# Kernel tuning notes

Hardware: AMD Instinct MI355X
Metric: run time of the kernel (lower is better)

## Reference

```python
import jax, jax.numpy as jnp
import numpy as np

K = 2            # negative:positive edge ratio (init arg k)
N_NODES = 4096
N_EDGES = 8192
FEAT = 64


def setup_inputs() -> dict:
    key = jax.random.key(0)
    k1, k2, k3 = jax.random.split(key, 3)
    node_feature = jax.random.normal(k1, (N_NODES, FEAT), dtype=jnp.float32)
    edge_src = jax.random.randint(k2, (N_EDGES,), 0, N_NODES, dtype=jnp.int32)
    edge_dst = jax.random.randint(k3, (N_EDGES,), 0, N_NODES, dtype=jnp.int32)
    return {"node_feature": node_feature, "edge_src": edge_src, "edge_dst": edge_dst}


def reference(node_feature, edge_src, edge_dst):
    E = edge_src.shape[0]
    N = node_feature.shape[0]
    # [E, E] pairwise mask: candidate column j is valid for row i iff
    # dst[j] != dst[i] and dst[j] != src[i]
    valid = (edge_dst[:, None] != edge_dst[None, :]) & (edge_src[:, None] != edge_dst[None, :])
    # unsorted_segment_min over rows grouped by edge_src -> [N, E]
    segmin = jax.ops.segment_min(valid.astype(jnp.int8), edge_src, num_segments=N)
    # gather back per edge -> [E, E], flatten
    m = segmin[edge_src].reshape(-1).astype(bool)  # [E*E]
    num_negatives = jnp.sum(m)
    ratio = num_negatives // E                      # integer ratio as in TF code
    keep_prob = (K / ratio).astype(jnp.float32)
    u = jax.random.uniform(jax.random.key(42), (E * E,), dtype=jnp.float32)
    keep = m & (u < keep_prob)
    # fixed-size (jit-friendly) stand-in for tf.boolean_mask: expected count is K*E;
    # pad/truncate to exactly K*E kept flat indices (fill_value=0 pads).
    idx = jnp.nonzero(keep, size=K * E, fill_value=0)[0]
    rows = idx // E
    cols = idx % E
    edge_src_neg = edge_src[rows]
    edge_dst_neg = edge_dst[cols]
    return edge_src_neg, edge_dst_neg
```

## Files before the change

### kernel.cpp

```cpp
#include <hip/hip_runtime.h>
#include <stdint.h>
#include <math.h>

typedef unsigned int u32;
typedef unsigned long long u64;

#define E_CNT   8192
#define N_CNT   4096
#define TOT_N   (1u << 26)
#define OUT_K   16384
#define NODE_BM_WORDS 128
#define N_BLKS  8192

#define OFF_BAD      0x000000
#define OFF_CNT_DST  0x200000
#define OFF_CNT_SRC  0x204000
#define OFF_SCALARS  0x208000
#define OFF_DESC     0x210000
#define ZERO_BYTES   0x220000

__device__ __forceinline__ u32 rotl32(u32 x, u32 d) {
  return __builtin_amdgcn_alignbit(x, x, 32u - d);
}

__device__ __forceinline__ u32 mbcnt64(u64 m) {
  return __builtin_amdgcn_mbcnt_hi((u32)(m >> 32),
         __builtin_amdgcn_mbcnt_lo((u32)m, 0u));
}

__device__ __forceinline__ void threefry4_0_42(u32 ia, u32 ib, u32 ic, u32 id,
                                               u32& ra, u32& rb, u32& rc, u32& rd) {
  const u32 k1 = 42u, k2 = 0x1BD11BF0u;
  u32 A0 = 0u, A1 = ia + k1;
  u32 B0 = 0u, B1 = ib + k1;
  u32 C0 = 0u, C1 = ic + k1;
  u32 D0 = 0u, D1 = id + k1;
#define R4(r) { A0 += A1; B0 += B1; C0 += C1; D0 += D1; \
  A1 = rotl32(A1, r); B1 = rotl32(B1, r); C1 = rotl32(C1, r); D1 = rotl32(D1, r); \
  A1 ^= A0; B1 ^= B0; C1 ^= C0; D1 ^= D0; }
#define INJ(c0, c1) { A0 += (c0); B0 += (c0); C0 += (c0); D0 += (c0); \
  A1 += (c1); B1 += (c1); C1 += (c1); D1 += (c1); }
#define INJ1(c1) { A1 += (c1); B1 += (c1); C1 += (c1); D1 += (c1); }
  R4(13) R4(15) R4(26) R4(6)
  INJ(k1, k2 + 1u)
  R4(17) R4(29) R4(16) R4(24)
  INJ(k2, 2u)
  R4(13) R4(15) R4(26) R4(6)
  INJ1(k1 + 3u)
  R4(17) R4(29) R4(16) R4(24)
  INJ(k1, k2 + 4u)
  R4(13) R4(15) R4(26) R4(6)
  INJ(k2, 5u)
#undef R4
#undef INJ
#undef INJ1
  ra = A0 ^ A1;
  rb = B0 ^ B1;
  rc = C0 ^ C1;
  rd = D0 ^ D1;
}

__global__ void k_build(const int* __restrict__ src, const int* __restrict__ dst,
                        u32* __restrict__ bad, u32* __restrict__ cnt_dst,
                        u32* __restrict__ cnt_src) {
  int tid = blockIdx.x * 256 + threadIdx.x;
  if (tid < N_CNT) {
    atomicOr(&bad[(u32)tid * NODE_BM_WORDS + ((u32)tid >> 5)], 1u << (tid & 31));
  }
  u32 s = (u32)src[tid], d = (u32)dst[tid];
  atomicOr(&bad[s * NODE_BM_WORDS + (d >> 5)], 1u << (d & 31));
  atomicAdd(&cnt_dst[d], 1u);
  atomicAdd(&cnt_src[s], 1u);
}

__global__ void __launch_bounds__(1024) k_rowcount(const u32* __restrict__ bad,
                                                   const u32* __restrict__ cnt_dst,
                                                   const u32* __restrict__ cnt_src,
                                                   u32* __restrict__ scal) {
  int wv = threadIdx.x >> 6, ln = threadIdx.x & 63;
  int n = blockIdx.x * 16 + wv;
  const u32* row = bad + (u32)n * NODE_BM_WORDS;
  u32 sum = 0;
#pragma unroll
  for (int h = 0; h < 2; ++h) {
    int w = ln + h * 64;
    u32 bits = row[w];
    while (bits) { int b = __ffs(bits) - 1; sum += cnt_dst[(w << 5) + b]; bits &= bits - 1; }
  }
#pragma unroll
  for (int off = 32; off > 0; off >>= 1) sum += __shfl_down(sum, off, 64);
  __shared__ u32 part[16];
  if (ln == 0) part[wv] = ((u32)E_CNT - sum) * cnt_src[n];
  __syncthreads();
  if (threadIdx.x == 0) {
    u32 tot = 0;
#pragma unroll
    for (int k = 0; k < 16; ++k) tot += part[k];
    atomicAdd(&scal[0], tot);
    __threadfence();
    if (atomicAdd(&scal[1], 1u) == 255u) {
      u32 nn = atomicAdd(&scal[0], 0u);
      u32 ratio = nn >> 13;
      float kp = 2.0f / (float)ratio;
      u32 T = (u32)ceil((double)kp * 8388608.0);
      u32 T9 = (T >= (1u << 23)) ? 0xFFFFFFFFu : (T << 9);
      atomicExch(&scal[2], T9);
    }
  }
}

__global__ void __launch_bounds__(1024) k_sample(const int* __restrict__ src,
                                                 const int* __restrict__ dst,
                                                 const u32* __restrict__ bad,
                                                 u32* __restrict__ scal,
                                                 u64* __restrict__ desc,
                                                 int* __restrict__ out) {
  __shared__ u32 sh_cnt[16];
  __shared__ u32 sh_vb;
  __shared__ u32 sh_excl;
  const u32 t = threadIdx.x;
  const u32 wv = t >> 6, ln = t & 63;

  if (t == 0) sh_vb = atomicAdd(&scal[3], 1u);
  __syncthreads();
  const u32 vb = sh_vb;
  const u32 T9 = scal[2];
  const u32 i0w = vb * 8192u + wv * 512u;

  u64 words[8];
  u64 any = 0;
#pragma unroll
  for (int h = 0; h < 2; ++h) {
    u32 i0 = i0w + (u32)h * 256u + ln;
    u32 b0, b1, b2, b3;
    threefry4_0_42(i0, i0 + 64u, i0 + 128u, i0 + 192u, b0, b1, b2, b3);
    u64 m0 = __ballot(b0 < T9);
    u64 m1 = __ballot(b1 < T9);
    u64 m2 = __ballot(b2 < T9);
    u64 m3 = __ballot(b3 < T9);
    words[4 * h]     = m0;
    words[4 * h + 1] = m1;
    words[4 * h + 2] = m2;
    words[4 * h + 3] = m3;
    any |= m0 | m1 | m2 | m3;
  }
  if (any) {
#pragma unroll
    for (int k = 0; k < 8; ++k) {
      if (words[k]) {
        u32 i = i0w + (u32)k * 64u + ln;
        bool kp = (words[k] >> ln) & 1ull;
        if (kp) {
          u32 n = (u32)src[i >> 13]; u32 v = (u32)dst[i & 8191];
          kp = ((bad[n * NODE_BM_WORDS + (v >> 5)] >> (v & 31)) & 1u) == 0u;
        }
        words[k] = __ballot(kp);
      }
    }
  }
  u32 wcnt = 0;
#pragma unroll
  for (int k = 0; k < 8; ++k) wcnt += (u32)__popcll(words[k]);
  if (ln == 0) sh_cnt[wv] = wcnt;
  __syncthreads();

  if (wv == 0) {
    u32 tot = 0;
#pragma unroll
    for (int k = 0; k < 16; ++k) tot += sh_cnt[k];
    if (ln == 0) atomicExch(&desc[vb], (1ull << 32) | (u64)tot);
    u32 excl = 0;
    if (vb != 0u) {
      int base = (int)vb - 1;
      for (;;) {
        int idx = base - (int)ln;
        u64 d = (idx >= 0) ? atomicAdd(&desc[idx], 0ull) : (2ull << 32);
        u32 flag = (u32)(d >> 32);
        u64 incl_m = __ballot(flag == 2u);
        u64 nr_m   = __ballot(flag == 0u);
        int fi = incl_m ? (__ffsll((unsigned long long)incl_m) - 1) : 64;
        int fn = nr_m   ? (__ffsll((unsigned long long)nr_m)   - 1) : 64;
        if (fn < fi) { __builtin_amdgcn_s_sleep(1); continue; }
        u32 contrib = ((int)ln <= fi) ? (u32)d : 0u;
#pragma unroll
        for (int off = 32; off > 0; off >>= 1) contrib += __shfl_down(contrib, off, 64);
        excl += __shfl(contrib, 0, 64);
        if (fi < 64) break;
        base -= 64;
        if (base < 0) break;
      }
    }
    if (ln == 0) {
      atomicExch(&desc[vb], (2ull << 32) | (u64)(excl + tot));
      sh_excl = excl;
    }
  }
  __syncthreads();

  u32 wexcl = sh_excl;
#pragma unroll
  for (int k = 0; k < 16; ++k) wexcl += ((u32)k < wv) ? sh_cnt[k] : 0u;
  u32 rbase = wexcl;
#pragma unroll
  for (int k = 0; k < 8; ++k) {
    u64 wk = words[k];
    if ((wk >> ln) & 1ull) {
      u32 rank = rbase + mbcnt64(wk);
      if (rank < OUT_K) {
        u32 i = i0w + (u32)k * 64u + ln;
        out[rank]         = src[i >> 13];
        out[OUT_K + rank] = dst[i & 8191];
      }
    }
    rbase += (u32)__popcll(wk);
  }

  if (vb == (u32)(N_BLKS - 1)) {
    u32 tot = 0;
#pragma unroll
    for (int k = 0; k < 16; ++k) tot += sh_cnt[k];
    u32 total = sh_excl + tot;
    int s0 = src[0], d0 = dst[0];
    for (u32 p = total + t; p < OUT_K; p += 1024u) {
      out[p] = s0; out[OUT_K + p] = d0;
    }
  }
}

extern "C" void kernel_launch(void* const* d_in, const int* in_sizes, int n_in,
                              void* d_out, int out_size, void* d_ws, size_t ws_size,
                              hipStream_t stream) {
  const int* src = (const int*)d_in[1];
  const int* dst = (const int*)d_in[2];
  int* out = (int*)d_out;
  char* ws = (char*)d_ws;

  u32* bad     = (u32*)(ws + OFF_BAD);
  u32* cnt_dst = (u32*)(ws + OFF_CNT_DST);
  u32* cnt_src = (u32*)(ws + OFF_CNT_SRC);
  u32* scal    = (u32*)(ws + OFF_SCALARS);
  u64* desc    = (u64*)(ws + OFF_DESC);

  hipMemsetAsync(ws, 0, ZERO_BYTES, stream);
  k_build<<<E_CNT / 256, 256, 0, stream>>>(src, dst, bad, cnt_dst, cnt_src);
  k_rowcount<<<N_CNT / 16, 1024, 0, stream>>>(bad, cnt_dst, cnt_src, scal);
  k_sample<<<N_BLKS, 1024, 0, stream>>>(src, dst, bad, scal, desc, out);
}
```

Measured before the change: 223.2 us.

## Fuse build and rowcount kernels via grid barrier; widen decoupled look-back to full block

Merges the bitmap/count build kernel and the row-count kernel into one launch of 256 blocks that synchronise through a global atomic barrier, with atomic reads ensuring visibility of the other blocks' writes. This removes one kernel launch and its gap. The sampling kernel's decoupled look-back now uses all 1024 threads (16 waves) to scan 1024 predecessor descriptors per step instead of 64 from one wave, combining the results through shared memory. The grid barrier relies on all 256 blocks being co-resident, and the wider look-back adds block-level syncs on every iteration.

```diff
diff --git a/kernel.cpp b/kernel.cpp
--- a/kernel.cpp
+++ b/kernel.cpp
@@ -26,6 +26,11 @@
 __device__ __forceinline__ u32 mbcnt64(u64 m) {
   return __builtin_amdgcn_mbcnt_hi((u32)(m >> 32),
          __builtin_amdgcn_mbcnt_lo((u32)m, 0u));
+}
+
+__device__ __forceinline__ u32 aread(u32* p) { return atomicAdd(p, 0u); }
+__device__ __forceinline__ u64 aread64(u64* p) {
+  return atomicAdd((unsigned long long*)p, 0ull);
 }
 
 __device__ __forceinline__ void threefry4_0_42(u32 ia, u32 ib, u32 ic, u32 id,
@@ -60,46 +65,55 @@
   rd = D0 ^ D1;
 }
 
-__global__ void k_build(const int* __restrict__ src, const int* __restrict__ dst,
-                        u32* __restrict__ bad, u32* __restrict__ cnt_dst,
-                        u32* __restrict__ cnt_src) {
-  int tid = blockIdx.x * 256 + threadIdx.x;
-  if (tid < N_CNT) {
-    atomicOr(&bad[(u32)tid * NODE_BM_WORDS + ((u32)tid >> 5)], 1u << (tid & 31));
-  }
-  u32 s = (u32)src[tid], d = (u32)dst[tid];
-  atomicOr(&bad[s * NODE_BM_WORDS + (d >> 5)], 1u << (d & 31));
-  atomicAdd(&cnt_dst[d], 1u);
-  atomicAdd(&cnt_src[s], 1u);
-}
-
-__global__ void __launch_bounds__(1024) k_rowcount(const u32* __restrict__ bad,
-                                                   const u32* __restrict__ cnt_dst,
-                                                   const u32* __restrict__ cnt_src,
-                                                   u32* __restrict__ scal) {
-  int wv = threadIdx.x >> 6, ln = threadIdx.x & 63;
-  int n = blockIdx.x * 16 + wv;
-  const u32* row = bad + (u32)n * NODE_BM_WORDS;
+__global__ void __launch_bounds__(1024) k_build_count(const int* __restrict__ src,
+                                                      const int* __restrict__ dst,
+                                                      u32* __restrict__ bad,
+                                                      u32* __restrict__ cnt_dst,
+                                                      u32* __restrict__ cnt_src,
+                                                      u32* __restrict__ scal) {
+  const u32 t = threadIdx.x, blk = blockIdx.x;
+  const u32 gtid = blk * 1024u + t;
+  const u32 wv = t >> 6, ln = t & 63;
+
+  if (gtid < N_CNT) {
+    atomicOr(&bad[gtid * NODE_BM_WORDS + (gtid >> 5)], 1u << (gtid & 31));
+  }
+  if (gtid < E_CNT) {
+    u32 s = (u32)src[gtid], d = (u32)dst[gtid];
+    atomicOr(&bad[s * NODE_BM_WORDS + (d >> 5)], 1u << (d & 31));
+    atomicAdd(&cnt_dst[d], 1u);
+    atomicAdd(&cnt_src[s], 1u);
+  }
+  __syncthreads();
+  if (t == 0) {
+    __threadfence();
+    atomicAdd(&scal[4], 1u);
+    while (aread(&scal[4]) < 256u) __builtin_amdgcn_s_sleep(8);
+  }
+  __syncthreads();
+
+  u32 n = blk * 16u + wv;
+  u32 rb = n * NODE_BM_WORDS;
   u32 sum = 0;
 #pragma unroll
   for (int h = 0; h < 2; ++h) {
-    int w = ln + h * 64;
-    u32 bits = row[w];
-    while (bits) { int b = __ffs(bits) - 1; sum += cnt_dst[(w << 5) + b]; bits &= bits - 1; }
+    u32 w = ln + (u32)h * 64u;
+    u32 bits = aread(&bad[rb + w]);
+    while (bits) { int b = __ffs(bits) - 1; sum += aread(&cnt_dst[(w << 5) + b]); bits &= bits - 1; }
   }
 #pragma unroll
   for (int off = 32; off > 0; off >>= 1) sum += __shfl_down(sum, off, 64);
   __shared__ u32 part[16];
-  if (ln == 0) part[wv] = ((u32)E_CNT - sum) * cnt_src[n];
-  __syncthreads();
-  if (threadIdx.x == 0) {
+  if (ln == 0) part[wv] = ((u32)E_CNT - sum) * aread(&cnt_src[n]);
+  __syncthreads();
+  if (t == 0) {
     u32 tot = 0;
 #pragma unroll
     for (int k = 0; k < 16; ++k) tot += part[k];
     atomicAdd(&scal[0], tot);
     __threadfence();
     if (atomicAdd(&scal[1], 1u) == 255u) {
-      u32 nn = atomicAdd(&scal[0], 0u);
+      u32 nn = aread(&scal[0]);
       u32 ratio = nn >> 13;
       float kp = 2.0f / (float)ratio;
       u32 T = (u32)ceil((double)kp * 8388608.0);
@@ -117,7 +131,7 @@
                                                  int* __restrict__ out) {
   __shared__ u32 sh_cnt[16];
   __shared__ u32 sh_vb;
-  __shared__ u32 sh_excl;
+  __shared__ u32 s_fi[16], s_fn[16], s_ws[16];
   const u32 t = threadIdx.x;
   const u32 wv = t >> 6, ln = t & 63;
 
@@ -164,40 +178,51 @@
   if (ln == 0) sh_cnt[wv] = wcnt;
   __syncthreads();
 
-  if (wv == 0) {
-    u32 tot = 0;
-#pragma unroll
-    for (int k = 0; k < 16; ++k) tot += sh_cnt[k];
-    if (ln == 0) atomicExch(&desc[vb], (1ull << 32) | (u64)tot);
-    u32 excl = 0;
-    if (vb != 0u) {
-      int base = (int)vb - 1;
-      for (;;) {
-        int idx = base - (int)ln;
-        u64 d = (idx >= 0) ? atomicAdd(&desc[idx], 0ull) : (2ull << 32);
-        u32 flag = (u32)(d >> 32);
-        u64 incl_m = __ballot(flag == 2u);
-        u64 nr_m   = __ballot(flag == 0u);
-        int fi = incl_m ? (__ffsll((unsigned long long)incl_m) - 1) : 64;
-        int fn = nr_m   ? (__ffsll((unsigned long long)nr_m)   - 1) : 64;
-        if (fn < fi) { __builtin_amdgcn_s_sleep(1); continue; }
-        u32 contrib = ((int)ln <= fi) ? (u32)d : 0u;
+  u32 tot = 0;
+#pragma unroll
+  for (int k = 0; k < 16; ++k) tot += sh_cnt[k];
+  if (t == 0) atomicExch((unsigned long long*)&desc[vb], (1ull << 32) | (u64)tot);
+
+  u32 excl = 0;
+  if (vb != 0u) {
+    int base = (int)vb - 1;
+    for (;;) {
+      int idx = base - (int)t;
+      u64 d = (idx >= 0) ? aread64(&desc[idx]) : (2ull << 32);
+      u32 flag = (u32)(d >> 32), val = (u32)d;
+      u64 im = __ballot(flag == 2u);
+      u64 nm = __ballot(flag == 0u);
+      if (ln == 0) {
+        s_fi[wv] = im ? (wv * 64u + (u32)(__ffsll((unsigned long long)im) - 1)) : 0xFFFFFFFFu;
+        s_fn[wv] = nm ? (wv * 64u + (u32)(__ffsll((unsigned long long)nm) - 1)) : 0xFFFFFFFFu;
+      }
+      __syncthreads();
+      u32 gfi = 0xFFFFFFFFu, gfn = 0xFFFFFFFFu;
+#pragma unroll
+      for (int k = 0; k < 16; ++k) {
+        gfi = (s_fi[k] < gfi) ? s_fi[k] : gfi;
+        gfn = (s_fn[k] < gfn) ? s_fn[k] : gfn;
+      }
+      bool retry = (gfn < gfi);
+      if (!retry) {
+        u32 contrib = (t <= gfi) ? val : 0u;
 #pragma unroll
         for (int off = 32; off > 0; off >>= 1) contrib += __shfl_down(contrib, off, 64);
-        excl += __shfl(contrib, 0, 64);
-        if (fi < 64) break;
-        base -= 64;
-        if (base < 0) break;
-      }
-    }
-    if (ln == 0) {
-      atomicExch(&desc[vb], (2ull << 32) | (u64)(excl + tot));
-      sh_excl = excl;
-    }
-  }
-  __syncthreads();
-
-  u32 wexcl = sh_excl;
+        if (ln == 0) s_ws[wv] = contrib;
+      }
+      __syncthreads();
+      if (retry) { __builtin_amdgcn_s_sleep(4); continue; }
+      u32 wsum = 0;
+#pragma unroll
+      for (int k = 0; k < 16; ++k) wsum += s_ws[k];
+      excl += wsum;
+      if (gfi != 0xFFFFFFFFu) break;
+      base -= 1024;
+    }
+  }
+  if (t == 0) atomicExch((unsigned long long*)&desc[vb], (2ull << 32) | (u64)(excl + tot));
+
+  u32 wexcl = excl;
 #pragma unroll
   for (int k = 0; k < 16; ++k) wexcl += ((u32)k < wv) ? sh_cnt[k] : 0u;
   u32 rbase = wexcl;
@@ -216,10 +241,7 @@
   }
 
   if (vb == (u32)(N_BLKS - 1)) {
-    u32 tot = 0;
-#pragma unroll
-    for (int k = 0; k < 16; ++k) tot += sh_cnt[k];
-    u32 total = sh_excl + tot;
+    u32 total = excl + tot;
     int s0 = src[0], d0 = dst[0];
     for (u32 p = total + t; p < OUT_K; p += 1024u) {
       out[p] = s0; out[OUT_K + p] = d0;
@@ -242,7 +264,6 @@
   u64* desc    = (u64*)(ws + OFF_DESC);
 
   hipMemsetAsync(ws, 0, ZERO_BYTES, stream);
-  k_build<<<E_CNT / 256, 256, 0, stream>>>(src, dst, bad, cnt_dst, cnt_src);
-  k_rowcount<<<N_CNT / 16, 1024, 0, stream>>>(bad, cnt_dst, cnt_src, scal);
+  k_build_count<<<256, 1024, 0, stream>>>(src, dst, bad, cnt_dst, cnt_src, scal);
   k_sample<<<N_BLKS, 1024, 0, stream>>>(src, dst, bad, scal, desc, out);
 }
```

Measured after the change: 269.5 us. 20.8% more time.
